# Kernel optimization log

Hardware: AMD Instinct MI355X
Metric: run time of the kernel (lower is better)

The kernel has to match this reference:

```python
import jax, jax.numpy as jnp
import numpy as np

NUM_NODES = 10000
D = 128      # input_dim (embedding dim)
N = 64       # visit_code_num
V = 50       # visit_thresh (time steps)
B = 256      # batch
H = 384      # hidden_dim
L = 8        # levels
CH = H // L  # chunk_size
K = 10       # conv_size (sliding window / conv kernel)
OUT = 128    # output_dim
ND = N * D


def setup_inputs() -> dict:
    key = jax.random.key(0)
    ks = jax.random.split(key, 16)
    node_ids = jax.random.randint(ks[0], (B, V, N), 0, NUM_NODES + 1)
    edge_idx = jax.random.randint(ks[1], (2, 4), 0, 100)
    edge_attr = jax.random.normal(ks[2], (4, 1), jnp.float32)
    visit_times = jax.random.uniform(ks[3], (B, V), jnp.float32)
    visit_order = jax.random.randint(ks[4], (B, V), 0, V)
    attn_mask = jnp.zeros((B, V, N), dtype=bool)
    embed = jax.random.normal(ks[5], (NUM_NODES + 1, D), jnp.float32) * 0.02
    embed = embed.at[0].set(0.0)  # padding_idx=0
    G = 4 * H + 2 * L
    Wk = jax.random.normal(ks[6], (G, ND + 1), jnp.float32) * 0.01
    bk = jnp.zeros((G,), jnp.float32)
    Wr = jax.random.normal(ks[7], (G, H + 1), jnp.float32) * 0.05
    br = jnp.zeros((G,), jnp.float32)
    Ws = jax.random.normal(ks[8], (H // 6, H), jnp.float32) * 0.05
    bs = jnp.zeros((H // 6,), jnp.float32)
    Wrs = jax.random.normal(ks[9], (H, H // 6), jnp.float32) * 0.05
    brs = jnp.zeros((H,), jnp.float32)
    Wc = jax.random.normal(ks[10], (H, H, K), jnp.float32) * 0.02  # Conv1d weight [out,in,k]
    bc = jnp.zeros((H,), jnp.float32)
    Wo = jax.random.normal(ks[11], (OUT, H), jnp.float32) * 0.05
    bo = jnp.zeros((OUT,), jnp.float32)
    return dict(node_ids=node_ids, edge_idx=edge_idx, edge_attr=edge_attr,
                visit_times=visit_times, visit_order=visit_order, attn_mask=attn_mask,
                embed=embed, Wk=Wk, bk=bk, Wr=Wr, br=br, Ws=Ws, bs=bs,
                Wrs=Wrs, brs=brs, Wc=Wc, bc=bc, Wo=Wo, bo=bo)


def _cumax_l2r(z):
    return jnp.cumsum(jax.nn.softmax(z, -1), -1)


def _cumax_r2l(z):
    s = jax.nn.softmax(z, -1)
    return jnp.flip(jnp.cumsum(jnp.flip(s, -1), -1), -1)


def _forward(node_ids, attn_mask, visit_times, embed, Wk, bk, Wr, br,
             Ws, bs, Wrs, brs, Wc, bc, Wo, bo):
    b, v, n = node_ids.shape
    # gather(expand(embed), node_ids) == plain embedding lookup
    x = embed[node_ids].reshape(b, v, n * D)  # [B,V,ND]

    def step(carry, xt):
        c, h, tmp_h, tmp_dis = carry
        inp, interval = xt
        xi = jnp.concatenate([inp, interval[:, None]], -1)   # [B,ND+1]
        hi = jnp.concatenate([h, interval[:, None]], -1)     # [B,H+1]
        xout = xi @ Wk.T + bk + hi @ Wr.T + br               # [B,4H+2L]
        fm = _cumax_l2r(xout[:, :L])[:, :, None]             # [B,L,1]
        im = _cumax_r2l(xout[:, L:2 * L])[:, :, None]        # [B,L,1]
        g = xout[:, 2 * L:].reshape(b, 4 * L, CH)
        f = jax.nn.sigmoid(g[:, :L])
        i = jax.nn.sigmoid(g[:, L:2 * L])
        o = jax.nn.sigmoid(g[:, 2 * L:3 * L])
        cin = jnp.tanh(g[:, 3 * L:])
        cl = c.reshape(b, L, CH)
        ov = fm * im
        c_new = ov * (f * cl + i * cin) + (fm - ov) * cl + (im - ov) * cin
        h_new = (o * jnp.tanh(c_new)).reshape(b, H)
        c_new = c_new.reshape(b, H)
        cur_dist = 1.0 - jnp.mean(fm[:, :, 0], -1)           # [B]
        tmp_h = jnp.concatenate([tmp_h[1:], h_new[None]], 0)        # [K,B,H]
        tmp_dis = jnp.concatenate([tmp_dis[1:], cur_dist[None]], 0)  # [K,B]
        local_dis = jax.nn.softmax(jnp.cumsum(tmp_dis.T, 1), 1)     # [B,K]
        local_h = tmp_h.transpose(1, 2, 0) * local_dis[:, None, :]  # [B,H,K]
        theme = jnp.mean(local_h, -1)                               # [B,H]
        theme = jax.nn.sigmoid(jax.nn.relu(theme @ Ws.T + bs) @ Wrs.T + brs)
        conv = jnp.einsum('bhk,ohk->bo', local_h, Wc) + bc          # Conv1d, out len 1
        return (c_new, h_new, tmp_h, tmp_dis), (h_new, theme * conv)

    carry0 = (jnp.zeros((b, H), x.dtype), jnp.zeros((b, H), x.dtype),
              jnp.zeros((K, b, H), x.dtype), jnp.zeros((K, b), x.dtype))
    _, (origin_h, hs) = jax.lax.scan(step, carry0,
                                     (x.transpose(1, 0, 2), visit_times.T))
    rnn = (hs + origin_h).transpose(1, 0, 2)   # [B,V,H]
    output = rnn @ Wo.T + bo                   # [B,V,OUT]
    visit_mask = jnp.all(attn_mask, -1)        # [B,V] True = padded visit
    last = jnp.sum((~visit_mask).astype(jnp.int32), -1) - 1
    return output[jnp.arange(b), last]         # [B,OUT] logits


def reference(node_ids, edge_idx, edge_attr, visit_times, visit_order, attn_mask,
              embed, Wk, bk, Wr, br, Ws, bs, Wrs, brs, Wc, bc, Wo, bo):
    return _forward(node_ids, attn_mask, visit_times, embed, Wk, bk, Wr, br,
                    Ws, bs, Wrs, brs, Wc, bc, Wo, bo)
```

## Files before the change

### kernel.cpp

```cpp
#include <hip/hip_runtime.h>
#include <stdint.h>


typedef unsigned short u16;
typedef short bf16x8 __attribute__((ext_vector_type(8)));
typedef float f32x4 __attribute__((ext_vector_type(4)));

#define GLL(gp, lp)                                                            \
  __builtin_amdgcn_global_load_lds(                                            \
      (const __attribute__((address_space(1))) unsigned int*)(gp),             \
      (__attribute__((address_space(3))) unsigned int*)(lp), 16, 0, 0)

__device__ __forceinline__ float bf2f(u16 u) {
  union { unsigned int i; float f; } v;
  v.i = ((unsigned int)u) << 16;
  return v.f;
}
__device__ __forceinline__ u16 f2bf(float f) {
  union { float f; unsigned int i; } v;
  v.f = f;
  unsigned int r = (v.i + 0x7fffu + ((v.i >> 16) & 1u)) >> 16;
  return (u16)r;
}
__device__ __forceinline__ float ldf(const void* p, size_t i, int isbf) {
  return isbf ? bf2f(((const u16*)p)[i]) : ((const float*)p)[i];
}
__device__ __forceinline__ float sigf(float x) { return 1.f / (1.f + __expf(-x)); }
__device__ __forceinline__ float tanhf_(float x) {
  float cx = fminf(fmaxf(x, -15.f), 15.f);
  float e = __expf(2.f * cx);
  return (e - 1.f) / (e + 1.f);
}
__device__ __forceinline__ float dot8_bf(const u16* w, const float* lp) {
  uint4 wv = *(const uint4*)w;
  union { unsigned int u; float f; } a0, a1;
  float s;
  a0.u = wv.x << 16; a1.u = wv.x & 0xffff0000u;
  s = lp[0] * a0.f + lp[1] * a1.f;
  a0.u = wv.y << 16; a1.u = wv.y & 0xffff0000u;
  s += lp[2] * a0.f + lp[3] * a1.f;
  a0.u = wv.z << 16; a1.u = wv.z & 0xffff0000u;
  s += lp[4] * a0.f + lp[5] * a1.f;
  a0.u = wv.w << 16; a1.u = wv.w & 0xffff0000u;
  s += lp[6] * a0.f + lp[7] * a1.f;
  return s;
}

__device__ __forceinline__ int gperm(int gp) {
  if (gp < 16) return gp;
  int r = gp - 16;
  int q = r & 3, h = r >> 2;
  return 16 + q * 384 + h;
}

__global__ void k_detect(const unsigned int* __restrict__ emb_raw,
                         int* __restrict__ flag) {
  if (blockIdx.x == 0 && threadIdx.x == 0) {
    int cnt = 0;
    for (int i = 64; i < 128; ++i) {
      unsigned int u = emb_raw[i];
      unsigned int lo = u & 0xffffu;
      unsigned int ex = (lo >> 7) & 0xffu;
      if (lo != 0 && ex >= 100 && ex <= 126) ++cnt;
    }
    *flag = (cnt >= 32) ? 1 : 0;
  }
}

__global__ void k_cvt_emb(const void* __restrict__ src, u16* __restrict__ dst,
                          const int* __restrict__ flagp) {
  int isbf = *flagp;
  int n = 10001 * 128;
  int i = blockIdx.x * blockDim.x + threadIdx.x;
  int stride = gridDim.x * blockDim.x;
  for (; i < n; i += stride)
    dst[i] = isbf ? ((const u16*)src)[i] : f2bf(((const float*)src)[i]);
}

__global__ void k_repack_wk(const void* __restrict__ wk, u16* __restrict__ wkp,
                            const int* __restrict__ flagp) {
  int isbf = *flagp;
  size_t i = (size_t)blockIdx.x * blockDim.x + threadIdx.x;
  size_t total = (size_t)1664 * 8192;
  size_t stride = (size_t)gridDim.x * blockDim.x;
  for (; i < total; i += stride) {
    size_t gp = i >> 13, k = i & 8191;
    u16 v = (u16)0;
    if (gp < 1552) {
      int g = gperm((int)gp);
      v = f2bf(ldf(wk, (size_t)g * 8193 + k, isbf));
    }
    wkp[i] = v;
  }
}

__global__ void k_prep_wr2(const void* __restrict__ wr, const void* __restrict__ wk,
                           const void* __restrict__ bk, const void* __restrict__ br,
                           u16* __restrict__ wrP2, float* __restrict__ biasC,
                           float* __restrict__ wlC, const int* __restrict__ flagp) {
  int isbf = *flagp;
  int i0 = blockIdx.x * blockDim.x + threadIdx.x;
  int stride = gridDim.x * blockDim.x;
  for (int j = i0; j < 1552 * 384; j += stride) {
    int gp = j / 384, k = j - gp * 384;
    int g = gperm(gp);
    wrP2[j] = f2bf(ldf(wr, (size_t)g * 385 + k, isbf));
  }
  for (int gp = i0; gp < 1552; gp += stride) {
    int g = gperm(gp);
    biasC[gp] = ldf(bk, g, isbf) + ldf(br, g, isbf);
    wlC[gp] = ldf(wk, (size_t)g * 8193 + 8192, isbf) + ldf(wr, g * 385 + 384, isbf);
  }
}

__global__ void k_repack_wc(const void* __restrict__ wc, u16* __restrict__ wcp,
                            const int* __restrict__ flagp) {
  int isbf = *flagp;
  int i0 = blockIdx.x * blockDim.x + threadIdx.x;
  int stride = gridDim.x * blockDim.x;
  for (int j = i0; j < 384 * 3840; j += stride) {
    int o = j / 3840;
    int r = j - o * 3840;
    int k = r / 384;
    int h = r - k * 384;
    wcp[j] = f2bf(ldf(wc, (o * 384 + h) * 10 + k, isbf));
  }
}

__global__ void k_cvt_smalls(const void* vt, const void* Ws, const void* bs,
                             const void* Wrs, const void* brs, const void* bc,
                             const void* Wo, const void* bo,
                             float* __restrict__ dst, const int* __restrict__ flagp) {
  int isbf = *flagp;
  int i = blockIdx.x * blockDim.x + threadIdx.x;
  int stride = gridDim.x * blockDim.x;
  for (; i < 112064; i += stride) {
    float v;
    if (i < 12800) v = ldf(vt, i, isbf);
    else if (i < 37376) v = ldf(Ws, i - 12800, isbf);
    else if (i < 37440) v = ldf(bs, i - 37376, isbf);
    else if (i < 62016) v = ldf(Wrs, i - 37440, isbf);
    else if (i < 62400) v = ldf(brs, i - 62016, isbf);
    else if (i < 62784) v = ldf(bc, i - 62400, isbf);
    else if (i < 111936) v = ldf(Wo, i - 62784, isbf);
    else v = ldf(bo, i - 111936, isbf);
    dst[i] = v;
  }
}

__global__ void k_zero(float* __restrict__ p, int n) {
  int i = blockIdx.x * blockDim.x + threadIdx.x;
  int stride = gridDim.x * blockDim.x;
  for (; i < n; i += stride) p[i] = 0.f;
}

__global__ __launch_bounds__(256) void k_gemm_xk(
    const int* __restrict__ node_ids, const u16* __restrict__ embB,
    const u16* __restrict__ wkp, const float* __restrict__ vtF,
    const float* __restrict__ biasC, const float* __restrict__ wlC,
    u16* __restrict__ xkb) {
  __shared__ alignas(16) u16 As[128 * 64];
  __shared__ alignas(16) u16 Bs[128 * 64];
  __shared__ alignas(16) u16 idS[128 * 66];
  int tid = threadIdx.x;
  int lin = blockIdx.x;
  int xcd = lin & 7, slot = lin >> 3;
  int job = (xcd < 4) ? (xcd * 163 + slot) : (4 * 163 + (xcd - 4) * 162 + slot);
  int mb = job % 100, gb = job / 100;
  int m0 = mb * 128;
  int g0 = gb * 128;
  int tq = m0 >> 8, b0t = m0 & 255;
  int lane = tid & 63, w = tid >> 6;
  int wy = w >> 1, wx = w & 1;
  f32x4 acc[4][4];
#pragma unroll
  for (int i = 0; i < 4; ++i)
#pragma unroll
    for (int j = 0; j < 4; ++j) acc[i][j] = (f32x4){0.f, 0.f, 0.f, 0.f};

  {
    const int4* nb = (const int4*)(node_ids + ((size_t)b0t * 50 + tq) * 64);
    for (int i = tid; i < 2048; i += 256) {
      int row = i >> 4, c4 = i & 15;
      int4 v = nb[(size_t)row * 800 + c4];
      u16* d = idS + row * 66 + c4 * 4;
      d[0] = (u16)v.x; d[1] = (u16)v.y; d[2] = (u16)v.z; d[3] = (u16)v.w;
    }
  }

  int l15 = lane & 15, lq = lane >> 4;
  int lr = lane >> 3, lc = lane & 7;
  int swc = (lc ^ lr) * 8;
  int cRd = (lq ^ (l15 & 7)) * 8;

  for (int kt = 0; kt < 128; ++kt) {
    __syncthreads();
#pragma unroll
    for (int c = 0; c < 4; ++c) {
      int chunk = w * 4 + c;
      int r = chunk * 8 + lr;
      int id = (int)idS[r * 66 + (kt >> 1)];
      const u16* gp = embB + (size_t)id * 128 + (kt & 1) * 64 + swc;
      u16* lp = As + chunk * 512 + lane * 8;
      GLL(gp, lp);
    }
#pragma unroll
    for (int c = 0; c < 4; ++c) {
      int chunk = w * 4 + c;
      int r = chunk * 8 + lr;
      const u16* gp = wkp + (size_t)(g0 + r) * 8192 + (size_t)kt * 64 + swc;
      u16* lp = Bs + chunk * 512 + lane * 8;
      GLL(gp, lp);
    }
    __syncthreads();
    const u16* Ab = As + (wy * 64 + l15) * 64;
    const u16* Bb = Bs + (wx * 64 + l15) * 64;
#pragma unroll
    for (int ks = 0; ks < 2; ++ks) {
      int co = cRd ^ (ks * 32);
      bf16x8 av[4], bv[4];
#pragma unroll
      for (int i = 0; i < 4; ++i) av[i] = *(const bf16x8*)(Ab + i * 1024 + co);
#pragma unroll
      for (int j = 0; j < 4; ++j) bv[j] = *(const bf16x8*)(Bb + j * 1024 + co);
#pragma unroll
      for (int i = 0; i < 4; ++i)
#pragma unroll
        for (int j = 0; j < 4; ++j)
          acc[i][j] =
              __builtin_amdgcn_mfma_f32_16x16x32_bf16(av[i], bv[j], acc[i][j], 0, 0, 0);
    }
  }
  float vt[4][4];
#pragma unroll
  for (int i = 0; i < 4; ++i)
#pragma unroll
    for (int p = 0; p < 4; ++p)
      vt[i][p] = vtF[(size_t)(b0t + wy * 64 + i * 16 + lq * 4 + p) * 50 + tq];
#pragma unroll
  for (int j = 0; j < 4; ++j) {
    int gcol = g0 + wx * 64 + j * 16 + l15;
    if (gcol < 1552) {
      float bC = biasC[gcol], wC = wlC[gcol];
#pragma unroll
      for (int i = 0; i < 4; ++i)
#pragma unroll
        for (int p = 0; p < 4; ++p) {
          int row = wy * 64 + i * 16 + lq * 4 + p;
          xkb[(size_t)(m0 + row) * 1552 + gcol] =
              f2bf(acc[i][j][p] + bC + vt[i][p] * wC);
        }
    }
  }
}

__global__ __launch_bounds__(512) void k_scan5(
    const u16* __restrict__ xkb,
    const u16* __restrict__ wrP2,
    float* __restrict__ hbuf,
    float* __restrict__ dbuf,
    unsigned int* __restrict__ hx,
    int* __restrict__ barCnt) {
  __shared__ alignas(16) u16 WrS[144 * 392];
  __shared__ alignas(16) u16 hS[16 * 392];
  __shared__ alignas(16) float fmTile[16 * 17];
  __shared__ float fmS[16][8], imS[16][8];

  int tid = threadIdx.x;
  int L = blockIdx.x;
  int xcd = L & 7, kk = L >> 3;
  int hi = (kk >= 12) ? 1 : 0;
  int bg = (xcd << 1) | hi;
  int gs = kk - 12 * hi;
  int b0 = bg * 16;
  int wv = tid >> 6, lane = tid & 63, l15 = lane & 15, lq = lane >> 4;

  for (int idx = tid; idx < 144 * 48; idx += 512) {
    int r = idx / 48, c = idx - r * 48;
    int gr = (r < 16) ? r : (16 + gs * 128 + (r - 16));
    *(uint4*)(WrS + r * 392 + c * 8) =
        *(const uint4*)(wrP2 + (size_t)gr * 384 + c * 8);
  }

  int hmy = gs * 32 + wv * 4 + lq;
  int lmy = hmy / 48;
  int bmy = b0 + l15;
  float creg = 0.f;

  const u16* arow_g = WrS + (16 + wv * 16 + l15) * 392 + lq * 8;
  const u16* arow_f = WrS + l15 * 392 + lq * 8;
  const u16* brow = hS + l15 * 392 + lq * 8;
  __syncthreads();

  for (int t = 0; t < 50; ++t) {
    uint2 xkg = *(const uint2*)(xkb + ((size_t)t * 256 + bmy) * 1552 + 16 +
                                gs * 128 + wv * 16 + lq * 4);
    uint4 xksm = (uint4){0u, 0u, 0u, 0u};
    if (tid < 32)
      xksm = *(const uint4*)(xkb + ((size_t)t * 256 + b0 + (tid & 15)) * 1552 +
                             ((tid < 16) ? 0 : 8));

    {
      const unsigned int* hxin = hx + (size_t)(t & 1) * 49152 + (size_t)b0 * 192;
#pragma unroll
      for (int k2 = 0; k2 < 6; ++k2) {
        int j = tid + k2 * 512;
        int r = j / 192, c = j - r * 192;
        unsigned int v = __hip_atomic_load(&hxin[r * 192 + c], __ATOMIC_RELAXED,
                                           __HIP_MEMORY_SCOPE_AGENT);
        *(unsigned int*)((char*)hS + r * 784 + c * 4) = v;
      }
    }
    __syncthreads();

    bf16x8 hb[12];
#pragma unroll
    for (int ks = 0; ks < 12; ++ks)
      hb[ks] = *(const bf16x8*)(brow + ks * 32);

    f32x4 accg = (f32x4){0.f, 0.f, 0.f, 0.f};
    f32x4 accf = (f32x4){0.f, 0.f, 0.f, 0.f};
#pragma unroll
    for (int ks = 0; ks < 12; ++ks) {
      bf16x8 ag = *(const bf16x8*)(arow_g + ks * 32);
      accg = __builtin_amdgcn_mfma_f32_16x16x32_bf16(ag, hb[ks], accg, 0, 0, 0);
      if (wv == 0) {
        bf16x8 a0 = *(const bf16x8*)(arow_f + ks * 32);
        accf = __builtin_amdgcn_mfma_f32_16x16x32_bf16(a0, hb[ks], accf, 0, 0, 0);
      }
    }
    if (wv == 0) {
#pragma unroll
      for (int p = 0; p < 4; ++p) fmTile[(lq * 4 + p) * 17 + l15] = accf[p];
    }
    __syncthreads();

    if (tid < 32) {
      int r = tid & 15;
      const u16* xs = (const u16*)&xksm;
      float z[8], m = -1e30f;
#pragma unroll
      for (int j = 0; j < 8; ++j) {
        int jj = (tid < 16) ? j : (8 + j);
        z[j] = fmTile[jj * 17 + r] + bf2f(xs[j]);
        m = fmaxf(m, z[j]);
      }
      float s = 0.f;
#pragma unroll
      for (int j = 0; j < 8; ++j) { z[j] = __expf(z[j] - m); s += z[j]; }
      float inv = 1.f / s;
      if (tid < 16) {
        float run = 0.f, fsum = 0.f;
#pragma unroll
        for (int j = 0; j < 8; ++j) { run += z[j] * inv; fmS[r][j] = run; fsum += run; }
        if (gs == 0) dbuf[(size_t)t * 256 + b0 + r] = 1.f - fsum * 0.125f;
      } else {
        float run = 0.f;
#pragma unroll
        for (int j = 7; j >= 0; --j) { run += z[j] * inv; imS[r][j] = run; }
      }
    }
    __syncthreads();

    {
      const u16* xg = (const u16*)&xkg;
      float x0 = accg[0] + bf2f(xg[0]);
      float x1 = accg[1] + bf2f(xg[1]);
      float x2 = accg[2] + bf2f(xg[2]);
      float x3 = accg[3] + bf2f(xg[3]);
      float fg = sigf(x0), ig = sigf(x1), og = sigf(x2), ci = tanhf_(x3);
      float fm = fmS[l15][lmy], im = imS[l15][lmy];
      float ov = fm * im;
      float cn = ov * (fg * creg + ig * ci) + (fm - ov) * creg + (im - ov) * ci;
      float hn = og * tanhf_(cn);
      creg = cn;
      hbuf[((size_t)t * 256 + bmy) * 384 + hmy] = hn;
      if (t != 49) {
        unsigned int v = (unsigned int)f2bf(hn);
        unsigned int up = __shfl_down(v, 16);
        if ((lq & 1) == 0) {
          unsigned int packed = v | (up << 16);
          __hip_atomic_store(
              &hx[(size_t)((t + 1) & 1) * 49152 + (size_t)bmy * 192 + gs * 16 +
                  wv * 2 + (lq >> 1)],
              packed, __ATOMIC_RELAXED, __HIP_MEMORY_SCOPE_AGENT);
        }
      }
    }

    if (t != 49) {
      asm volatile("s_waitcnt vmcnt(0)" ::: "memory");
      __syncthreads();
      if (tid == 0) {
        __hip_atomic_fetch_add(&barCnt[bg], 1, __ATOMIC_RELAXED,
                               __HIP_MEMORY_SCOPE_AGENT);
        while (__hip_atomic_load(&barCnt[bg], __ATOMIC_RELAXED,
                                 __HIP_MEMORY_SCOPE_AGENT) < 12 * (t + 1)) {
          __builtin_amdgcn_s_sleep(1);
        }
      }
      __syncthreads();
    }
  }
}

__global__ __launch_bounds__(384) void k_final(
    const float* __restrict__ hbuf, const float* __restrict__ dbuf,
    const unsigned char* __restrict__ am, const float* __restrict__ smalls,
    const u16* __restrict__ wcp, float* __restrict__ out) {
  const float* WsF = smalls + 12800;
  const float* bsF = smalls + 37376;
  const float* WrsF = smalls + 37440;
  const float* brsF = smalls + 62016;
  const float* bcF = smalls + 62400;
  const float* WoF = smalls + 62784;
  const float* boF = smalls + 111936;
  __shared__ alignas(16) float lh2[10][384];
  __shared__ alignas(16) float ti[384];
  __shared__ alignas(16) float us[64];
  __shared__ alignas(16) float rnnS[384];
  __shared__ alignas(16) float hlastS[384];
  __shared__ float ldS[10];
  __shared__ int npad[50];
  __shared__ int lastS;
  int tid = threadIdx.x;
  int b = blockIdx.x;

  if (tid < 50) {
    const unsigned char* mr = am + ((size_t)b * 50 + tid) * 64;
    int all1 = 1;
    for (int q = 0; q < 64; ++q) all1 &= (mr[q] != 0);
    npad[tid] = all1 ? 0 : 1;
  }
  __syncthreads();
  if (tid == 0) {
    int c = 0;
    for (int v = 0; v < 50; ++v) c += npad[v];
    int lv = c - 1;
    int last = lv < 0 ? 0 : lv;
    lastS = last;
    float cum = 0.f, cv[10];
    for (int k = 0; k < 10; ++k) {
      int s = last - 9 + k;
      float dk = (s >= 0) ? dbuf[(size_t)s * 256 + b] : 0.f;
      cum += dk;
      cv[k] = cum;
    }
    float m = cv[0];
    for (int k = 1; k < 10; ++k) m = fmaxf(m, cv[k]);
    float ssum = 0.f, ee[10];
    for (int k = 0; k < 10; ++k) { ee[k] = __expf(cv[k] - m); ssum += ee[k]; }
    float inv = 1.f / ssum;
    for (int k = 0; k < 10; ++k) ldS[k] = ee[k] * inv;
  }
  __syncthreads();
  {
    int h = tid;
    int last = lastS;
    float ssum = 0.f;
    for (int k = 0; k < 10; ++k) {
      int s = last - 9 + k;
      float hv = (s >= 0) ? hbuf[((size_t)s * 256 + b) * 384 + h] : 0.f;
      float v = hv * ldS[k];
      lh2[k][h] = v;
      ssum += v;
    }
    ti[h] = ssum * 0.1f;
    hlastS[h] = hbuf[((size_t)last * 256 + b) * 384 + h];
  }
  __syncthreads();
  if (tid < 64) {
    float a = bsF[tid];
    const float* wr = WsF + (size_t)tid * 384;
    for (int h = 0; h < 384; ++h) a += wr[h] * ti[h];
    us[tid] = fmaxf(a, 0.f);
  }
  __syncthreads();
  {
    int o = tid;
    float th = brsF[o];
    const float* wr = WrsF + (size_t)o * 64;
    for (int k = 0; k < 64; ++k) th += wr[k] * us[k];
    th = sigf(th);
    float cacc = bcF[o];
    for (int k = 0; k < 10; ++k) {
      const u16* wrow = wcp + ((size_t)o * 10 + k) * 384;
      const float* lrow = lh2[k];
      for (int h8 = 0; h8 < 48; ++h8) cacc += dot8_bf(wrow + h8 * 8, lrow + h8 * 8);
    }
    rnnS[o] = th * cacc + hlastS[o];
  }
  __syncthreads();
  if (tid < 128) {
    float a = boF[tid];
    const float* wr = WoF + (size_t)tid * 384;
    for (int h = 0; h < 384; ++h) a += wr[h] * rnnS[h];
    out[(size_t)b * 128 + tid] = a;
  }
}

extern "C" void kernel_launch(void* const* d_in, const int* in_sizes, int n_in,
                              void* d_out, int out_size, void* d_ws, size_t ws_size,
                              hipStream_t stream) {
  const int* node_ids = (const int*)d_in[0];
  const void* vtR = d_in[3];
  const unsigned char* am = (const unsigned char*)d_in[5];
  const void* embR = d_in[6];
  const void* WkR = d_in[7];
  const void* bkR = d_in[8];
  const void* WrR = d_in[9];
  const void* brR = d_in[10];
  const void* WsR = d_in[11];
  const void* bsR = d_in[12];
  const void* WrsR = d_in[13];
  const void* brsR = d_in[14];
  const void* WcR = d_in[15];
  const void* bcR = d_in[16];
  const void* WoR = d_in[17];
  const void* boR = d_in[18];
  (void)in_sizes; (void)n_in; (void)out_size; (void)ws_size;

  char* ws = (char*)d_ws;
  size_t off = 0;
  auto alloc = [&](size_t bytes) {
    void* p = ws + off;
    off = (off + bytes + 255) & ~(size_t)255;
    return p;
  };
  int* flagp = (int*)alloc(4);
  u16* embB = (u16*)alloc((size_t)10001 * 128 * 2);
  u16* WkP = (u16*)alloc((size_t)1664 * 8192 * 2);
  u16* WrP2 = (u16*)alloc((size_t)1552 * 384 * 2);
  float* biasC = (float*)alloc(1552 * 4);
  float* wlC = (float*)alloc(1552 * 4);
  float* smalls = (float*)alloc((size_t)112064 * 4);
  u16* XKb = (u16*)alloc((size_t)12800 * 1552 * 2);
  u16* WcP = (u16*)alloc((size_t)384 * 3840 * 2);
  float* Hbuf = (float*)alloc((size_t)50 * 256 * 384 * 4);
  float* Dbuf = (float*)alloc((size_t)50 * 256 * 4);
  unsigned int* Hx = (unsigned int*)alloc((size_t)2 * 256 * 192 * 4);
  int* BarCnt = (int*)alloc(16 * 4);

  k_detect<<<dim3(1), dim3(64), 0, stream>>>((const unsigned int*)embR, flagp);
  k_cvt_emb<<<dim3(1024), dim3(256), 0, stream>>>(embR, embB, flagp);
  k_repack_wk<<<dim3(2048), dim3(256), 0, stream>>>(WkR, WkP, flagp);
  k_prep_wr2<<<dim3(512), dim3(256), 0, stream>>>(WrR, WkR, bkR, brR, WrP2, biasC,
                                                  wlC, flagp);
  k_repack_wc<<<dim3(512), dim3(256), 0, stream>>>(WcR, WcP, flagp);
  k_cvt_smalls<<<dim3(128), dim3(256), 0, stream>>>(vtR, WsR, bsR, WrsR, brsR,
                                                    bcR, WoR, boR, smalls, flagp);
  k_zero<<<dim3(96), dim3(256), 0, stream>>>((float*)Hx, 98304);
  k_zero<<<dim3(1), dim3(64), 0, stream>>>((float*)BarCnt, 16);

  k_gemm_xk<<<dim3(1300), dim3(256), 0, stream>>>(node_ids, embB, WkP, smalls,
                                                  biasC, wlC, XKb);

  k_scan5<<<dim3(192), dim3(512), 0, stream>>>(XKb, WrP2, Hbuf, Dbuf, Hx, BarCnt);

  k_final<<<dim3(256), dim3(384), 0, stream>>>(Hbuf, Dbuf, am, smalls, WcP,
                                               (float*)d_out);
}
```

Before: 993.2 us.

## Enlarge input-projection GEMM tiles to 256x256 with 512-thread blocks

Moves the embedding-gather GEMM from 128x128 tiles with 256 threads to 256x256 tiles with 512 threads (8 waves, 128x64 per wave), and pads the packed Wk to 1792 rows to match. Each M tile now covers exactly one time step across the whole batch. Node ids are read straight from global memory into registers every other k-step instead of being staged in shared memory first. The larger tiles increase reuse of each loaded A and B tile and cut the number of blocks. The cost is 350 blocks on a machine with many CUs, doubled accumulator registers, more wasted work in the padded G dimension, and small scattered id loads sitting on the k-loop critical path.

Measured after the change: 1.103 ms. 1.11x slower.

```diff
diff --git a/kernel.cpp b/kernel.cpp
--- a/kernel.cpp
+++ b/kernel.cpp
@@ -81,7 +81,7 @@
                             const int* __restrict__ flagp) {
   int isbf = *flagp;
   size_t i = (size_t)blockIdx.x * blockDim.x + threadIdx.x;
-  size_t total = (size_t)1664 * 8192;
+  size_t total = (size_t)1792 * 8192;
   size_t stride = (size_t)gridDim.x * blockDim.x;
   for (; i < total; i += stride) {
     size_t gp = i >> 13, k = i & 8191;
@@ -154,99 +154,94 @@
   for (; i < n; i += stride) p[i] = 0.f;
 }
 
-__global__ __launch_bounds__(256) void k_gemm_xk(
+__global__ __launch_bounds__(512, 2) void k_gemm_xk(
     const int* __restrict__ node_ids, const u16* __restrict__ embB,
     const u16* __restrict__ wkp, const float* __restrict__ vtF,
     const float* __restrict__ biasC, const float* __restrict__ wlC,
     u16* __restrict__ xkb) {
-  __shared__ alignas(16) u16 As[128 * 64];
-  __shared__ alignas(16) u16 Bs[128 * 64];
-  __shared__ alignas(16) u16 idS[128 * 66];
+  __shared__ alignas(16) u16 As[256 * 64];
+  __shared__ alignas(16) u16 Bs[256 * 64];
   int tid = threadIdx.x;
   int lin = blockIdx.x;
   int xcd = lin & 7, slot = lin >> 3;
-  int job = (xcd < 4) ? (xcd * 163 + slot) : (4 * 163 + (xcd - 4) * 162 + slot);
-  int mb = job % 100, gb = job / 100;
-  int m0 = mb * 128;
-  int g0 = gb * 128;
-  int tq = m0 >> 8, b0t = m0 & 255;
+  int job = (xcd < 6) ? (xcd * 44 + slot) : (264 + (xcd - 6) * 43 + slot);
+  int gb = job / 50, mb = job % 50;
+  int m0 = mb * 256;
+  int g0 = gb * 256;
+  int tq = mb;
   int lane = tid & 63, w = tid >> 6;
-  int wy = w >> 1, wx = w & 1;
-  f32x4 acc[4][4];
-#pragma unroll
-  for (int i = 0; i < 4; ++i)
+  int wy = w >> 2, wx = w & 3;
+  f32x4 acc[8][4];
+#pragma unroll
+  for (int i = 0; i < 8; ++i)
 #pragma unroll
     for (int j = 0; j < 4; ++j) acc[i][j] = (f32x4){0.f, 0.f, 0.f, 0.f};
-
-  {
-    const int4* nb = (const int4*)(node_ids + ((size_t)b0t * 50 + tq) * 64);
-    for (int i = tid; i < 2048; i += 256) {
-      int row = i >> 4, c4 = i & 15;
-      int4 v = nb[(size_t)row * 800 + c4];
-      u16* d = idS + row * 66 + c4 * 4;
-      d[0] = (u16)v.x; d[1] = (u16)v.y; d[2] = (u16)v.z; d[3] = (u16)v.w;
-    }
-  }
 
   int l15 = lane & 15, lq = lane >> 4;
   int lr = lane >> 3, lc = lane & 7;
   int swc = (lc ^ lr) * 8;
   int cRd = (lq ^ (l15 & 7)) * 8;
 
+  int rowA[4];
+#pragma unroll
+  for (int c = 0; c < 4; ++c) rowA[c] = (w * 4 + c) * 8 + lr;
+  int id4[4];
+
   for (int kt = 0; kt < 128; ++kt) {
+    if (!(kt & 1)) {
+#pragma unroll
+      for (int c = 0; c < 4; ++c)
+        id4[c] = node_ids[((size_t)rowA[c] * 50 + tq) * 64 + (kt >> 1)];
+    }
     __syncthreads();
 #pragma unroll
     for (int c = 0; c < 4; ++c) {
       int chunk = w * 4 + c;
-      int r = chunk * 8 + lr;
-      int id = (int)idS[r * 66 + (kt >> 1)];
-      const u16* gp = embB + (size_t)id * 128 + (kt & 1) * 64 + swc;
-      u16* lp = As + chunk * 512 + lane * 8;
-      GLL(gp, lp);
+      const u16* gp = embB + (size_t)id4[c] * 128 + (kt & 1) * 64 + swc;
+      GLL(gp, As + chunk * 512 + lane * 8);
     }
 #pragma unroll
     for (int c = 0; c < 4; ++c) {
       int chunk = w * 4 + c;
       int r = chunk * 8 + lr;
       const u16* gp = wkp + (size_t)(g0 + r) * 8192 + (size_t)kt * 64 + swc;
-      u16* lp = Bs + chunk * 512 + lane * 8;
-      GLL(gp, lp);
+      GLL(gp, Bs + chunk * 512 + lane * 8);
     }
     __syncthreads();
-    const u16* Ab = As + (wy * 64 + l15) * 64;
+    const u16* Ab = As + (wy * 128 + l15) * 64;
     const u16* Bb = Bs + (wx * 64 + l15) * 64;
 #pragma unroll
     for (int ks = 0; ks < 2; ++ks) {
       int co = cRd ^ (ks * 32);
-      bf16x8 av[4], bv[4];
-#pragma unroll
-      for (int i = 0; i < 4; ++i) av[i] = *(const bf16x8*)(Ab + i * 1024 + co);
+      bf16x8 av[8], bv[4];
+#pragma unroll
+      for (int i = 0; i < 8; ++i) av[i] = *(const bf16x8*)(Ab + i * 1024 + co);
 #pragma unroll
       for (int j = 0; j < 4; ++j) bv[j] = *(const bf16x8*)(Bb + j * 1024 + co);
 #pragma unroll
-      for (int i = 0; i < 4; ++i)
+      for (int i = 0; i < 8; ++i)
 #pragma unroll
         for (int j = 0; j < 4; ++j)
           acc[i][j] =
               __builtin_amdgcn_mfma_f32_16x16x32_bf16(av[i], bv[j], acc[i][j], 0, 0, 0);
     }
   }
-  float vt[4][4];
-#pragma unroll
-  for (int i = 0; i < 4; ++i)
+  float vt[8][4];
+#pragma unroll
+  for (int i = 0; i < 8; ++i)
 #pragma unroll
     for (int p = 0; p < 4; ++p)
-      vt[i][p] = vtF[(size_t)(b0t + wy * 64 + i * 16 + lq * 4 + p) * 50 + tq];
+      vt[i][p] = vtF[(size_t)(wy * 128 + i * 16 + lq * 4 + p) * 50 + tq];
 #pragma unroll
   for (int j = 0; j < 4; ++j) {
     int gcol = g0 + wx * 64 + j * 16 + l15;
     if (gcol < 1552) {
       float bC = biasC[gcol], wC = wlC[gcol];
 #pragma unroll
-      for (int i = 0; i < 4; ++i)
+      for (int i = 0; i < 8; ++i)
 #pragma unroll
         for (int p = 0; p < 4; ++p) {
-          int row = wy * 64 + i * 16 + lq * 4 + p;
+          int row = wy * 128 + i * 16 + lq * 4 + p;
           xkb[(size_t)(m0 + row) * 1552 + gcol] =
               f2bf(acc[i][j][p] + bC + vt[i][p] * wC);
         }
@@ -529,7 +524,7 @@
   };
   int* flagp = (int*)alloc(4);
   u16* embB = (u16*)alloc((size_t)10001 * 128 * 2);
-  u16* WkP = (u16*)alloc((size_t)1664 * 8192 * 2);
+  u16* WkP = (u16*)alloc((size_t)1792 * 8192 * 2);
   u16* WrP2 = (u16*)alloc((size_t)1552 * 384 * 2);
   float* biasC = (float*)alloc(1552 * 4);
   float* wlC = (float*)alloc(1552 * 4);
@@ -552,8 +547,8 @@
   k_zero<<<dim3(96), dim3(256), 0, stream>>>((float*)Hx, 98304);
   k_zero<<<dim3(1), dim3(64), 0, stream>>>((float*)BarCnt, 16);
 
-  k_gemm_xk<<<dim3(1300), dim3(256), 0, stream>>>(node_ids, embB, WkP, smalls,
-                                                  biasC, wlC, XKb);
+  k_gemm_xk<<<dim3(350), dim3(512), 0, stream>>>(node_ids, embB, WkP, smalls,
+                                                 biasC, wlC, XKb);
 
   k_scan5<<<dim3(192), dim3(512), 0, stream>>>(XKb, WrP2, Hbuf, Dbuf, Hx, BarCnt);
 
```

## Compute cumax gates redundantly per wave with shuffles, defer hbuf stores

Applied to the files above, without the earlier changes.

Every wave now computes the 16-wide master-gate MFMA and its softmax/cumsum itself, using cross-lane shuffles instead of one wave writing an LDS tile and 32 threads doing the cumax. This removes two __syncthreads and the LDS round trips from each serial timestep. The hbuf/dbuf global stores are deferred by one step so they overlap the next step's hx load instead of sitting before the inter-block barrier's vmcnt wait. The cost is extra MFMA and exp work duplicated across all eight waves.

Measured after the change: 961.3 us. -3.2%, faster.

```diff
diff --git a/kernel.cpp b/kernel.cpp
--- a/kernel.cpp
+++ b/kernel.cpp
@@ -254,7 +254,7 @@
   }
 }
 
-__global__ __launch_bounds__(512) void k_scan5(
+__global__ __launch_bounds__(512) void k_scan6(
     const u16* __restrict__ xkb,
     const u16* __restrict__ wrP2,
     float* __restrict__ hbuf,
@@ -263,8 +263,6 @@
     int* __restrict__ barCnt) {
   __shared__ alignas(16) u16 WrS[144 * 392];
   __shared__ alignas(16) u16 hS[16 * 392];
-  __shared__ alignas(16) float fmTile[16 * 17];
-  __shared__ float fmS[16][8], imS[16][8];
 
   int tid = threadIdx.x;
   int L = blockIdx.x;
@@ -283,9 +281,10 @@
   }
 
   int hmy = gs * 32 + wv * 4 + lq;
-  int lmy = hmy / 48;
+  int lmy = (gs * 32 + wv * 4) / 48;
   int bmy = b0 + l15;
   float creg = 0.f;
+  float hbufPend = 0.f, dvalPend = 0.f;
 
   const u16* arow_g = WrS + (16 + wv * 16 + l15) * 392 + lq * 8;
   const u16* arow_f = WrS + l15 * 392 + lq * 8;
@@ -293,12 +292,9 @@
   __syncthreads();
 
   for (int t = 0; t < 50; ++t) {
-    uint2 xkg = *(const uint2*)(xkb + ((size_t)t * 256 + bmy) * 1552 + 16 +
-                                gs * 128 + wv * 16 + lq * 4);
-    uint4 xksm = (uint4){0u, 0u, 0u, 0u};
-    if (tid < 32)
-      xksm = *(const uint4*)(xkb + ((size_t)t * 256 + b0 + (tid & 15)) * 1552 +
-                             ((tid < 16) ? 0 : 8));
+    const u16* xkrow = xkb + ((size_t)t * 256 + bmy) * 1552;
+    uint2 xkg = *(const uint2*)(xkrow + 16 + gs * 128 + wv * 16 + lq * 4);
+    uint2 xkf = *(const uint2*)(xkrow + lq * 4);
 
     {
       const unsigned int* hxin = hx + (size_t)(t & 1) * 49152 + (size_t)b0 * 192;
@@ -311,6 +307,12 @@
         *(unsigned int*)((char*)hS + r * 784 + c * 4) = v;
       }
     }
+
+    if (t > 0) {
+      hbuf[((size_t)(t - 1) * 256 + bmy) * 384 + hmy] = hbufPend;
+      if (gs == 0 && wv == 0 && lq == 0)
+        dbuf[(size_t)(t - 1) * 256 + b0 + l15] = dvalPend;
+    }
     __syncthreads();
 
     bf16x8 hb[12];
@@ -323,44 +325,52 @@
 #pragma unroll
     for (int ks = 0; ks < 12; ++ks) {
       bf16x8 ag = *(const bf16x8*)(arow_g + ks * 32);
+      bf16x8 a0 = *(const bf16x8*)(arow_f + ks * 32);
       accg = __builtin_amdgcn_mfma_f32_16x16x32_bf16(ag, hb[ks], accg, 0, 0, 0);
-      if (wv == 0) {
-        bf16x8 a0 = *(const bf16x8*)(arow_f + ks * 32);
-        accf = __builtin_amdgcn_mfma_f32_16x16x32_bf16(a0, hb[ks], accf, 0, 0, 0);
+      accf = __builtin_amdgcn_mfma_f32_16x16x32_bf16(a0, hb[ks], accf, 0, 0, 0);
+    }
+
+    float dval;
+    float fmv, imv;
+    {
+      const u16* xf = (const u16*)&xkf;
+      float z0 = accf[0] + bf2f(xf[0]);
+      float z1 = accf[1] + bf2f(xf[1]);
+      float z2 = accf[2] + bf2f(xf[2]);
+      float z3 = accf[3] + bf2f(xf[3]);
+      float m4 = fmaxf(fmaxf(z0, z1), fmaxf(z2, z3));
+      float mm = fmaxf(m4, __shfl_xor(m4, 16));
+      float e0 = __expf(z0 - mm), e1 = __expf(z1 - mm);
+      float e2 = __expf(z2 - mm), e3 = __expf(z3 - mm);
+      float s4 = e0 + e1 + e2 + e3;
+      float so = __shfl_xor(s4, 16);
+      float inv = 1.f / (s4 + so);
+      float cum0, cum1, cum2, cum3;
+      if (lq < 2) {
+        float base = (lq == 1) ? so : 0.f;
+        cum0 = (base + e0) * inv;
+        cum1 = (base + e0 + e1) * inv;
+        cum2 = (base + e0 + e1 + e2) * inv;
+        cum3 = (base + s4) * inv;
+      } else {
+        float base = (lq == 2) ? so : 0.f;
+        cum3 = (base + e3) * inv;
+        cum2 = (base + e3 + e2) * inv;
+        cum1 = (base + e3 + e2 + e1) * inv;
+        cum0 = (base + s4) * inv;
       }
-    }
-    if (wv == 0) {
-#pragma unroll
-      for (int p = 0; p < 4; ++p) fmTile[(lq * 4 + p) * 17 + l15] = accf[p];
-    }
-    __syncthreads();
-
-    if (tid < 32) {
-      int r = tid & 15;
-      const u16* xs = (const u16*)&xksm;
-      float z[8], m = -1e30f;
-#pragma unroll
-      for (int j = 0; j < 8; ++j) {
-        int jj = (tid < 16) ? j : (8 + j);
-        z[j] = fmTile[jj * 17 + r] + bf2f(xs[j]);
-        m = fmaxf(m, z[j]);
-      }
-      float s = 0.f;
-#pragma unroll
-      for (int j = 0; j < 8; ++j) { z[j] = __expf(z[j] - m); s += z[j]; }
-      float inv = 1.f / s;
-      if (tid < 16) {
-        float run = 0.f, fsum = 0.f;
-#pragma unroll
-        for (int j = 0; j < 8; ++j) { run += z[j] * inv; fmS[r][j] = run; fsum += run; }
-        if (gs == 0) dbuf[(size_t)t * 256 + b0 + r] = 1.f - fsum * 0.125f;
-      } else {
-        float run = 0.f;
-#pragma unroll
-        for (int j = 7; j >= 0; --j) { run += z[j] * inv; imS[r][j] = run; }
-      }
-    }
-    __syncthreads();
+      float fs4 = cum0 + cum1 + cum2 + cum3;
+      float fst = fs4 + __shfl_xor(fs4, 16);
+      dval = 1.f - fst * 0.125f;
+      int r2 = lmy & 3;
+      float vsel = cum0;
+      if (r2 == 1) vsel = cum1;
+      else if (r2 == 2) vsel = cum2;
+      else if (r2 == 3) vsel = cum3;
+      int srcBase = l15 + ((lmy >> 2) << 4);
+      fmv = __shfl(vsel, srcBase);
+      imv = __shfl(vsel, srcBase + 32);
+    }
 
     {
       const u16* xg = (const u16*)&xkg;
@@ -369,12 +379,12 @@
       float x2 = accg[2] + bf2f(xg[2]);
       float x3 = accg[3] + bf2f(xg[3]);
       float fg = sigf(x0), ig = sigf(x1), og = sigf(x2), ci = tanhf_(x3);
-      float fm = fmS[l15][lmy], im = imS[l15][lmy];
-      float ov = fm * im;
-      float cn = ov * (fg * creg + ig * ci) + (fm - ov) * creg + (im - ov) * ci;
+      float ov = fmv * imv;
+      float cn = ov * (fg * creg + ig * ci) + (fmv - ov) * creg + (imv - ov) * ci;
       float hn = og * tanhf_(cn);
       creg = cn;
-      hbuf[((size_t)t * 256 + bmy) * 384 + hmy] = hn;
+      hbufPend = hn;
+      dvalPend = dval;
       if (t != 49) {
         unsigned int v = (unsigned int)f2bf(hn);
         unsigned int up = __shfl_down(v, 16);
@@ -402,6 +412,8 @@
       __syncthreads();
     }
   }
+  hbuf[((size_t)49 * 256 + bmy) * 384 + hmy] = hbufPend;
+  if (gs == 0 && wv == 0 && lq == 0) dbuf[(size_t)49 * 256 + b0 + l15] = dvalPend;
 }
 
 __global__ __launch_bounds__(384) void k_final(
@@ -555,7 +567,7 @@
   k_gemm_xk<<<dim3(1300), dim3(256), 0, stream>>>(node_ids, embB, WkP, smalls,
                                                   biasC, wlC, XKb);
 
-  k_scan5<<<dim3(192), dim3(512), 0, stream>>>(XKb, WrP2, Hbuf, Dbuf, Hx, BarCnt);
+  k_scan6<<<dim3(192), dim3(512), 0, stream>>>(XKb, WrP2, Hbuf, Dbuf, Hx, BarCnt);
 
   k_final<<<dim3(256), dim3(384), 0, stream>>>(Hbuf, Dbuf, am, smalls, WcP,
                                                (float*)d_out);
```
